# Optimization experiments

Hardware: AMD Instinct MI355X
Metric: run time of the kernel (lower is better)

Reference implementation:

```python
import jax, jax.numpy as jnp
import numpy as np

POOL_H, POOL_W = 7, 7


def _crop_and_resize(fmap, boxes, ph, pw):
    # TF tf.image.crop_and_resize (bilinear) semantics, vectorized over all boxes.
    # fmap: [B, H, W, C]; boxes: [B, N, 4] normalized (y1, x1, y2, x2)
    B, H, W, C = fmap.shape
    dt = fmap.dtype
    y1, x1, y2, x2 = (boxes[..., i] for i in range(4))  # each [B, N]
    iy = jnp.arange(ph, dtype=dt)
    ix = jnp.arange(pw, dtype=dt)
    # in_y = y1*(H-1) + i*(y2-y1)*(H-1)/(ph-1)
    ys = y1[..., None] * (H - 1) + iy * ((y2 - y1) * (H - 1) / (ph - 1))[..., None]  # [B,N,ph]
    xs = x1[..., None] * (W - 1) + ix * ((x2 - x1) * (W - 1) / (pw - 1))[..., None]  # [B,N,pw]
    y0f = jnp.floor(ys)
    x0f = jnp.floor(xs)
    y0 = jnp.clip(y0f.astype(jnp.int32), 0, H - 1)
    y1i = jnp.clip(y0 + 1, 0, H - 1)
    x0 = jnp.clip(x0f.astype(jnp.int32), 0, W - 1)
    x1i = jnp.clip(x0 + 1, 0, W - 1)
    fy = (ys - y0f)[:, :, :, None, None]  # [B,N,ph,1,1]
    fx = (xs - x0f)[:, :, None, :, None]  # [B,N,1,pw,1]

    def gather(fb, yi, xi):  # fb [H,W,C], yi [N,ph], xi [N,pw] -> [N,ph,pw,C]
        return fb[yi[:, :, None], xi[:, None, :]]

    g = jax.vmap(gather)
    tl = g(fmap, y0, x0)
    tr = g(fmap, y0, x1i)
    bl = g(fmap, y1i, x0)
    br = g(fmap, y1i, x1i)
    top = tl + (tr - tl) * fx
    bot = bl + (br - bl) * fx
    return top + (bot - top) * fy  # [B,N,ph,pw,C]


def setup_inputs() -> dict:
    key = jax.random.key(0)
    kb, k2, k3, k4, k5 = jax.random.split(key, 5)
    B, N, C = 2, 1000, 256
    # random well-formed boxes: two corners sorted per axis
    pts = jax.random.uniform(kb, (B, N, 2, 2), dtype=jnp.float32)
    lo = jnp.min(pts, axis=2)  # [B,N,2] -> (y, x) mins
    hi = jnp.max(pts, axis=2)
    boxes = jnp.stack([lo[..., 0], lo[..., 1], hi[..., 0], hi[..., 1]], axis=-1)
    # image_meta per compose_image_meta: image_shape lives at [:, 4:7]
    image_meta = jnp.zeros((B, 14), dtype=jnp.float32)
    image_meta = image_meta.at[:, 4].set(1024.0).at[:, 5].set(1024.0).at[:, 6].set(3.0)
    feat2 = jax.random.normal(k2, (B, 256, 256, C), dtype=jnp.float32)
    feat3 = jax.random.normal(k3, (B, 128, 128, C), dtype=jnp.float32)
    feat4 = jax.random.normal(k4, (B, 64, 64, C), dtype=jnp.float32)
    feat5 = jax.random.normal(k5, (B, 32, 32, C), dtype=jnp.float32)
    return {"boxes": boxes, "image_meta": image_meta, "feat2": feat2,
            "feat3": feat3, "feat4": feat4, "feat5": feat5}


def reference(boxes, image_meta, feat2, feat3, feat4, feat5):
    boxes = jax.lax.stop_gradient(boxes)  # matches tf.stop_gradient on level_boxes
    h = boxes[..., 2] - boxes[..., 0]  # [B,N]
    w = boxes[..., 3] - boxes[..., 1]
    img_shape = image_meta[0, 4:7]
    image_area = img_shape[0] * img_shape[1]
    lvl = jnp.log2(jnp.sqrt(h * w) / (224.0 / jnp.sqrt(image_area)))
    roi_level = jnp.clip(4.0 + jnp.round(lvl), 2.0, 5.0).astype(jnp.int32)  # [B,N]
    out = jnp.zeros(boxes.shape[:2] + (POOL_H, POOL_W, feat2.shape[-1]), dtype=feat2.dtype)
    for i, fm in enumerate((feat2, feat3, feat4, feat5)):
        crop = _crop_and_resize(fm, boxes, POOL_H, POOL_W)
        sel = (roi_level == (i + 2))[:, :, None, None, None]
        out = out + jnp.where(sel, crop, jnp.zeros((), dtype=crop.dtype))
    return out
```

## Files before the change

### kernel.cpp

```cpp
#include <hip/hip_runtime.h>


__global__ __launch_bounds__(64) void roi_align_kernel(
    const float* __restrict__ boxes,
    const float* __restrict__ meta,
    const float* __restrict__ f2,
    const float* __restrict__ f3,
    const float* __restrict__ f4,
    const float* __restrict__ f5,
    float* __restrict__ out,
    int N)
{
    const int C = 256;
    int cell = blockIdx.x;
    int bn   = cell / 49;
    int pc   = cell - bn * 49;
    int py   = pc / 7;
    int px   = pc - py * 7;
    int b    = bn / N;

    float y1 = boxes[bn * 4 + 0];
    float x1 = boxes[bn * 4 + 1];
    float y2 = boxes[bn * 4 + 2];
    float x2 = boxes[bn * 4 + 3];
    float h = y2 - y1;
    float w = x2 - x1;

    float area = meta[4] * meta[5];
    float lvl  = log2f(sqrtf(h * w) / (224.0f / sqrtf(area)));
    float rl   = 4.0f + rintf(lvl);
    rl = fminf(fmaxf(rl, 2.0f), 5.0f);
    int level = (int)rl;

    const float* fm;
    int H;
    if (level == 2)      { fm = f2; H = 256; }
    else if (level == 3) { fm = f3; H = 128; }
    else if (level == 4) { fm = f4; H = 64;  }
    else                 { fm = f5; H = 32;  }
    int W = H;

    float sy = (h * (float)(H - 1)) / 6.0f;
    float sx = (w * (float)(W - 1)) / 6.0f;
    float ys = y1 * (float)(H - 1) + (float)py * sy;
    float xs = x1 * (float)(W - 1) + (float)px * sx;
    float y0f = floorf(ys);
    float x0f = floorf(xs);
    int y0 = min(max((int)y0f, 0), H - 1);
    int yi = min(y0 + 1, H - 1);
    int x0 = min(max((int)x0f, 0), W - 1);
    int xi = min(x0 + 1, W - 1);
    float fy = ys - y0f;
    float fx = xs - x0f;

    size_t base = (size_t)b * H * W * C;
    const float4* ptl = (const float4*)(fm + base + ((size_t)y0 * W + x0) * C);
    const float4* ptr = (const float4*)(fm + base + ((size_t)y0 * W + xi) * C);
    const float4* pbl = (const float4*)(fm + base + ((size_t)yi * W + x0) * C);
    const float4* pbr = (const float4*)(fm + base + ((size_t)yi * W + xi) * C);

    int t = threadIdx.x;
    float4 tl = ptl[t];
    float4 tr = ptr[t];
    float4 bl = pbl[t];
    float4 br = pbr[t];

    float4 o;
    {
        float top = tl.x + (tr.x - tl.x) * fx;
        float bot = bl.x + (br.x - bl.x) * fx;
        o.x = top + (bot - top) * fy;
    }
    {
        float top = tl.y + (tr.y - tl.y) * fx;
        float bot = bl.y + (br.y - bl.y) * fx;
        o.y = top + (bot - top) * fy;
    }
    {
        float top = tl.z + (tr.z - tl.z) * fx;
        float bot = bl.z + (br.z - bl.z) * fx;
        o.z = top + (bot - top) * fy;
    }
    {
        float top = tl.w + (tr.w - tl.w) * fx;
        float bot = bl.w + (br.w - bl.w) * fx;
        o.w = top + (bot - top) * fy;
    }

    float4* po = (float4*)(out + (size_t)cell * C);
    po[t] = o;
}

extern "C" void kernel_launch(void* const* d_in, const int* in_sizes, int n_in,
                              void* d_out, int out_size, void* d_ws, size_t ws_size,
                              hipStream_t stream) {
    const float* boxes = (const float*)d_in[0];
    const float* meta  = (const float*)d_in[1];
    const float* f2    = (const float*)d_in[2];
    const float* f3    = (const float*)d_in[3];
    const float* f4    = (const float*)d_in[4];
    const float* f5    = (const float*)d_in[5];
    float* out = (float*)d_out;

    int B = in_sizes[1] / 14;
    int N = in_sizes[0] / (4 * B);

    int grid = B * N * 49;
    roi_align_kernel<<<grid, 64, 0, stream>>>(boxes, meta, f2, f3, f4, f5, out, N);
}
```

Before: 249.8 us.

## Process one box per 256-thread block, two cells per wave, nontemporal stores

Changes the work decomposition from one 64-thread block per output cell to one 256-thread block per box. Each of the four waves loops over cells and issues loads for two cells before interpolating, which adds memory-level parallelism per wave. Box and level setup is now done once per box instead of once per cell. Outputs are written with nontemporal stores so they do not pollute the cache. The price is fewer blocks and a serial loop per wave, which lowers the total number of resident waves available to hide memory latency.

```diff
diff --git a/kernel.cpp b/kernel.cpp
--- a/kernel.cpp
+++ b/kernel.cpp
@@ -1,23 +1,23 @@
 #include <hip/hip_runtime.h>
 
 
-__global__ __launch_bounds__(64) void roi_align_kernel(
+typedef float f4 __attribute__((ext_vector_type(4)));
+
+__global__ __launch_bounds__(256, 8) void roi_align_kernel(
     const float* __restrict__ boxes,
     const float* __restrict__ meta,
     const float* __restrict__ f2,
     const float* __restrict__ f3,
-    const float* __restrict__ f4,
+    const float* __restrict__ f4_,
     const float* __restrict__ f5,
     float* __restrict__ out,
     int N)
 {
     const int C = 256;
-    int cell = blockIdx.x;
-    int bn   = cell / 49;
-    int pc   = cell - bn * 49;
-    int py   = pc / 7;
-    int px   = pc - py * 7;
+    int bn   = blockIdx.x;
     int b    = bn / N;
+    int wave = threadIdx.x >> 6;
+    int lane = threadIdx.x & 63;
 
     float y1 = boxes[bn * 4 + 0];
     float x1 = boxes[bn * 4 + 1];
@@ -28,67 +28,82 @@
 
     float area = meta[4] * meta[5];
     float lvl  = log2f(sqrtf(h * w) / (224.0f / sqrtf(area)));
-    float rl   = 4.0f + rintf(lvl);
-    rl = fminf(fmaxf(rl, 2.0f), 5.0f);
-    int level = (int)rl;
+    float rl   = fminf(fmaxf(4.0f + rintf(lvl), 2.0f), 5.0f);
+    int level  = (int)rl;
 
     const float* fm;
     int H;
-    if (level == 2)      { fm = f2; H = 256; }
-    else if (level == 3) { fm = f3; H = 128; }
-    else if (level == 4) { fm = f4; H = 64;  }
-    else                 { fm = f5; H = 32;  }
-    int W = H;
+    if (level == 2)      { fm = f2;  H = 256; }
+    else if (level == 3) { fm = f3;  H = 128; }
+    else if (level == 4) { fm = f4_; H = 64;  }
+    else                 { fm = f5;  H = 32;  }
+    const int W = H;
 
-    float sy = (h * (float)(H - 1)) / 6.0f;
-    float sx = (w * (float)(W - 1)) / 6.0f;
-    float ys = y1 * (float)(H - 1) + (float)py * sy;
-    float xs = x1 * (float)(W - 1) + (float)px * sx;
-    float y0f = floorf(ys);
-    float x0f = floorf(xs);
-    int y0 = min(max((int)y0f, 0), H - 1);
-    int yi = min(y0 + 1, H - 1);
-    int x0 = min(max((int)x0f, 0), W - 1);
-    int xi = min(x0 + 1, W - 1);
-    float fy = ys - y0f;
-    float fx = xs - x0f;
+    float Hm1 = (float)(H - 1);
+    float sy = (h * Hm1) / 6.0f;
+    float sx = (w * Hm1) / 6.0f;
+    float yb = y1 * Hm1;
+    float xb = x1 * Hm1;
 
-    size_t base = (size_t)b * H * W * C;
-    const float4* ptl = (const float4*)(fm + base + ((size_t)y0 * W + x0) * C);
-    const float4* ptr = (const float4*)(fm + base + ((size_t)y0 * W + xi) * C);
-    const float4* pbl = (const float4*)(fm + base + ((size_t)yi * W + x0) * C);
-    const float4* pbr = (const float4*)(fm + base + ((size_t)yi * W + xi) * C);
+    const float* fmb  = fm  + (size_t)b  * H * W * C + lane * 4;
+    float*       outb = out + (size_t)bn * 49 * C    + lane * 4;
 
-    int t = threadIdx.x;
-    float4 tl = ptl[t];
-    float4 tr = ptr[t];
-    float4 bl = pbl[t];
-    float4 br = pbr[t];
+    auto cell_setup = [&](int c, const f4*& tl, const f4*& tr,
+                          const f4*& bl, const f4*& br, float& fx, float& fy) {
+        int py = c / 7;
+        int px = c - py * 7;
+        float ys = yb + (float)py * sy;
+        float xs = xb + (float)px * sx;
+        float y0f = floorf(ys);
+        float x0f = floorf(xs);
+        fy = ys - y0f;
+        fx = xs - x0f;
+        int y0 = min(max((int)y0f, 0), H - 1);
+        int x0 = min(max((int)x0f, 0), W - 1);
+        int yi = min(y0 + 1, H - 1);
+        int xi = min(x0 + 1, W - 1);
+        tl = (const f4*)(fmb + (y0 * W + x0) * C);
+        tr = (const f4*)(fmb + (y0 * W + xi) * C);
+        bl = (const f4*)(fmb + (yi * W + x0) * C);
+        br = (const f4*)(fmb + (yi * W + xi) * C);
+    };
 
-    float4 o;
-    {
-        float top = tl.x + (tr.x - tl.x) * fx;
-        float bot = bl.x + (br.x - bl.x) * fx;
-        o.x = top + (bot - top) * fy;
+    auto lerp4 = [](f4 tl, f4 tr, f4 bl, f4 br, float fx, float fy) {
+        f4 top = tl + (tr - tl) * fx;
+        f4 bot = bl + (br - bl) * fx;
+        return top + (bot - top) * fy;
+    };
+
+    #pragma unroll 1
+    for (int i = 0; i < 7; ++i) {
+        int cA = wave + i * 8;
+        int cB = cA + 4;
+        bool doA = (cA < 49);
+        bool doB = (cB < 49);
+
+        f4 tlA{}, trA{}, blA{}, brA{}, tlB{}, trB{}, blB{}, brB{};
+        float fxA = 0.f, fyA = 0.f, fxB = 0.f, fyB = 0.f;
+
+        if (doA) {
+            const f4 *ptl, *ptr_, *pbl, *pbr;
+            cell_setup(cA, ptl, ptr_, pbl, pbr, fxA, fyA);
+            tlA = *ptl; trA = *ptr_; blA = *pbl; brA = *pbr;
+        }
+        if (doB) {
+            const f4 *ptl, *ptr_, *pbl, *pbr;
+            cell_setup(cB, ptl, ptr_, pbl, pbr, fxB, fyB);
+            tlB = *ptl; trB = *ptr_; blB = *pbl; brB = *pbr;
+        }
+
+        if (doA) {
+            f4 o = lerp4(tlA, trA, blA, brA, fxA, fyA);
+            __builtin_nontemporal_store(o, (f4*)(outb + cA * C));
+        }
+        if (doB) {
+            f4 o = lerp4(tlB, trB, blB, brB, fxB, fyB);
+            __builtin_nontemporal_store(o, (f4*)(outb + cB * C));
+        }
     }
-    {
-        float top = tl.y + (tr.y - tl.y) * fx;
-        float bot = bl.y + (br.y - bl.y) * fx;
-        o.y = top + (bot - top) * fy;
-    }
-    {
-        float top = tl.z + (tr.z - tl.z) * fx;
-        float bot = bl.z + (br.z - bl.z) * fx;
-        o.z = top + (bot - top) * fy;
-    }
-    {
-        float top = tl.w + (tr.w - tl.w) * fx;
-        float bot = bl.w + (br.w - bl.w) * fx;
-        o.w = top + (bot - top) * fy;
-    }
-
-    float4* po = (float4*)(out + (size_t)cell * C);
-    po[t] = o;
 }
 
 extern "C" void kernel_launch(void* const* d_in, const int* in_sizes, int n_in,
@@ -98,13 +113,13 @@
     const float* meta  = (const float*)d_in[1];
     const float* f2    = (const float*)d_in[2];
     const float* f3    = (const float*)d_in[3];
-    const float* f4    = (const float*)d_in[4];
+    const float* f4_   = (const float*)d_in[4];
     const float* f5    = (const float*)d_in[5];
     float* out = (float*)d_out;
 
     int B = in_sizes[1] / 14;
     int N = in_sizes[0] / (4 * B);
 
-    int grid = B * N * 49;
-    roi_align_kernel<<<grid, 64, 0, stream>>>(boxes, meta, f2, f3, f4, f5, out, N);
+    int grid = B * N;
+    roi_align_kernel<<<grid, 256, 0, stream>>>(boxes, meta, f2, f3, f4_, f5, out, N);
 }
```

Result: slower. 258.6 us (+3.5%).
